# Performance work log

Measured on AMD Instinct MI355X. Metric: run time of the kernel, lower is better.

## Reference

```python
import jax, jax.numpy as jnp
import numpy as np

B, N, D = 4, 4096, 512          # batch, seq_len, hidden_size
H, DH = 8, 64                    # n_heads, head_dim
M = 512                          # nb_features = 0.125 * seq_len
LN_EPS = 1e-12
KERNEL_EPS = 1e-4


def setup_inputs() -> dict:
    key = jax.random.key(0)
    ks = jax.random.split(key, 12)
    s = 0.02
    return {
        "input_tensor": jax.random.normal(ks[0], (B, N, D), jnp.float32),
        "attention_mask": jnp.zeros((B, 1, 1, N), jnp.float32),  # unused by module
        "Wq": jax.random.normal(ks[1], (D, D), jnp.float32) * s,
        "bq": jnp.zeros((D,), jnp.float32),
        "Wk": jax.random.normal(ks[2], (D, D), jnp.float32) * s,
        "bk": jnp.zeros((D,), jnp.float32),
        "Wv": jax.random.normal(ks[3], (D, D), jnp.float32) * s,
        "bv": jnp.zeros((D,), jnp.float32),
        # gaussian (orthogonal-style) random feature projections [M, DH]
        "proj_q": jax.random.normal(ks[4], (M, DH), jnp.float32),
        "proj_k": jax.random.normal(ks[5], (M, DH), jnp.float32),
        "Wd": jax.random.normal(ks[6], (D, D), jnp.float32) * s,
        "bd": jnp.zeros((D,), jnp.float32),
        "gamma": jnp.ones((D,), jnp.float32),
        "beta": jnp.zeros((D,), jnp.float32),
    }


def _softmax_kernel(data, projection_matrix, is_query):
    # data: [B,H,N,DH], projection_matrix: [M,DH]
    data_normalizer = data.shape[-1] ** (-0.25)
    ratio = projection_matrix.shape[0] ** (-0.5)
    data_dash = jnp.einsum("bhnd,md->bhnm", data_normalizer * data, projection_matrix)
    diag_data = (jnp.sum(data * data, axis=-1) * 0.5 * data_normalizer ** 2)[..., None]
    if is_query:
        stab = jnp.max(data_dash, axis=-1, keepdims=True)
    else:
        stab = jnp.max(data_dash)  # global max, per original code
    return ratio * (jnp.exp(data_dash - diag_data - stab) + KERNEL_EPS)


def _linear_attention(q, k, v):
    # q,k: [B,H,N,M]; v: [B,H,N,DH]
    k_cumsum = jnp.sum(k, axis=-2)                               # [B,H,M]
    d_inv = 1.0 / jnp.einsum("bhnm,bhm->bhn", q, k_cumsum)       # [B,H,N]
    context = jnp.einsum("bhnm,bhne->bhme", k, v)                # [B,H,M,DH]
    return jnp.einsum("bhme,bhnm,bhn->bhne", context, q, d_inv)  # [B,H,N,DH]


def reference(input_tensor, attention_mask, Wq, bq, Wk, bk, Wv, bv,
              proj_q, proj_k, Wd, bd, gamma, beta):
    def heads(x):  # [B,N,D] -> [B,H,N,DH]
        return x.reshape(B, N, H, DH).transpose(0, 2, 1, 3)

    q = heads(input_tensor @ Wq.T + bq)
    k = heads(input_tensor @ Wk.T + bk)
    v = heads(input_tensor @ Wv.T + bv)

    q = _softmax_kernel(q, proj_q, is_query=True)
    k = _softmax_kernel(k, proj_k, is_query=False)

    ctx = _linear_attention(q, k, v)                  # [B,H,N,DH]
    ctx = ctx.transpose(0, 2, 1, 3).reshape(B, N, D)  # merge heads

    hidden = ctx @ Wd.T + bd                          # dropout is identity (eval)
    x = hidden + input_tensor
    mu = jnp.mean(x, axis=-1, keepdims=True)
    var = jnp.mean((x - mu) ** 2, axis=-1, keepdims=True)
    return (x - mu) / jnp.sqrt(var + LN_EPS) * gamma + beta
```

## Files before the change

### kernel.cpp

```cpp
#include <hip/hip_runtime.h>
#include <math.h>

typedef __bf16 bf16;
typedef __bf16 bf16x8 __attribute__((ext_vector_type(8)));
typedef __bf16 bf16x4 __attribute__((ext_vector_type(4)));
typedef float  f32x4  __attribute__((ext_vector_type(4)));

#define NSEQ 4096
#define DMODEL 512
#define DHEAD 64
#define MFEAT 512
#define BHEADS 32
#define ROWS_TOTAL 16384

#define NORMALIZER 0.35355339059327373f
#define DIAG_C 0.0625f
#define KEPS 1e-4f

__device__ __forceinline__ float warpReduceSum(float v) {
#pragma unroll
    for (int off = 32; off > 0; off >>= 1) v += __shfl_xor(v, off);
    return v;
}

__device__ __forceinline__ void atomicMaxF(float* addr, float val) {
    int* ai = (int*)addr;
    int cur = __float_as_int(*addr);
    while (__int_as_float(cur) < val) {
        int prev = atomicCAS(ai, cur, __float_as_int(val));
        if (prev == cur) break;
        cur = prev;
    }
}

__device__ __forceinline__ void gload16(const void* g, void* l) {
    __builtin_amdgcn_global_load_lds((const __attribute__((address_space(1))) void*)g,
                                     (__attribute__((address_space(3))) void*)l, 16, 0, 0);
}

__global__ __launch_bounds__(256)
void prep_convert(const float* __restrict__ x, const float* __restrict__ Wq,
                  const float* __restrict__ Wk, const float* __restrict__ Wv,
                  const float* __restrict__ Wd, const float* __restrict__ pq,
                  const float* __restrict__ bq, const float* __restrict__ bk,
                  const float* __restrict__ bv,
                  bf16* __restrict__ xb, bf16* __restrict__ Wb,
                  bf16* __restrict__ Wdb, bf16* __restrict__ pqb,
                  float* __restrict__ bcat)
{
    size_t i4 = (size_t)blockIdx.x * 256 + threadIdx.x;
    size_t e0 = i4 * 4;
    if (e0 >= 9471488) return;
    const float* src;
    if (e0 < 8388608) {
        src = x + e0;
        float4 v = *(const float4*)src;
        bf16* d = xb + e0;
        d[0] = (bf16)v.x; d[1] = (bf16)v.y; d[2] = (bf16)v.z; d[3] = (bf16)v.w;
    } else if (e0 < 9175040) {
        size_t c = e0 - 8388608; int wsel = (int)(c >> 18); size_t o = c & 262143;
        src = (wsel == 0 ? Wq : wsel == 1 ? Wk : Wv) + o;
        float4 v = *(const float4*)src;
        bf16* d = Wb + c;
        d[0] = (bf16)v.x; d[1] = (bf16)v.y; d[2] = (bf16)v.z; d[3] = (bf16)v.w;
    } else if (e0 < 9437184) {
        size_t c = e0 - 9175040;
        src = Wd + c;
        float4 v = *(const float4*)src;
        bf16* d = Wdb + c;
        d[0] = (bf16)v.x; d[1] = (bf16)v.y; d[2] = (bf16)v.z; d[3] = (bf16)v.w;
    } else if (e0 < 9469952) {
        size_t c = e0 - 9437184;
        src = pq + c;
        float4 v = *(const float4*)src;
        const int feat = (int)(c >> 6), col = (int)(c & 63);
        bf16x4 d4;
        d4[0] = (bf16)v.x; d4[1] = (bf16)v.y; d4[2] = (bf16)v.z; d4[3] = (bf16)v.w;
        const int inrow = (col << 1) ^ ((feat & 7) << 4);
        *(bf16x4*)((char*)pqb + (size_t)feat * 128 + inrow) = d4;
    } else {
        size_t c = e0 - 9469952; int wsel = (int)(c >> 9); size_t o = c & 511;
        src = (wsel == 0 ? bq : wsel == 1 ? bk : bv) + o;
        *(float4*)(bcat + c) = *(const float4*)src;
    }
}

template<int MODE>
__global__ __launch_bounds__(256)
void gemm_mfma(const bf16* __restrict__ A, const bf16* __restrict__ Bw,
               const float* __restrict__ bias, const float* __restrict__ resid,
               bf16* __restrict__ outQ, bf16* __restrict__ outK,
               bf16* __restrict__ outV, float* __restrict__ outF)
{
    __shared__ char As[16384];
    __shared__ char Bs[16384];
    const int tid = threadIdx.x;
    const int w = tid >> 6, l = tid & 63;
    const int wr = w >> 1, wc = w & 1;
    const int row0 = blockIdx.y << 7;
    const int col0 = blockIdx.x << 7;

    f32x4 acc[4][4] = {};
    const char* Ab = (const char*)A + (size_t)row0 * 1024;
    const char* Bb = (const char*)Bw + (size_t)col0 * 1024;

    for (int kt = 0; kt < 8; ++kt) {
        const int k0b = kt << 7;
#pragma unroll
        for (int i = 0; i < 4; ++i) {
            int off = (i << 12) + (tid << 4);
            int g = off ^ ((off >> 3) & 0x70);
            int grow = g >> 7, gcol = g & 127;
            gload16(Ab + (size_t)grow * 1024 + k0b + gcol, As + (i << 12) + (w << 10));
            gload16(Bb + (size_t)grow * 1024 + k0b + gcol, Bs + (i << 12) + (w << 10));
        }
        __syncthreads();
#pragma unroll
        for (int ks = 0; ks < 2; ++ks) {
            bf16x8 af[4], bb[4];
#pragma unroll
            for (int mi = 0; mi < 4; ++mi) {
                int row = (wr << 6) + (mi << 4) + (l & 15);
                int addr = ((row << 7) + (ks << 6) + ((l >> 4) << 4)) ^ ((row & 7) << 4);
                af[mi] = *(const bf16x8*)(As + addr);
            }
#pragma unroll
            for (int nj = 0; nj < 4; ++nj) {
                int row = (wc << 6) + (nj << 4) + (l & 15);
                int addr = ((row << 7) + (ks << 6) + ((l >> 4) << 4)) ^ ((row & 7) << 4);
                bb[nj] = *(const bf16x8*)(Bs + addr);
            }
#pragma unroll
            for (int mi = 0; mi < 4; ++mi)
#pragma unroll
                for (int nj = 0; nj < 4; ++nj)
                    acc[mi][nj] = __builtin_amdgcn_mfma_f32_16x16x32_bf16(af[mi], bb[nj], acc[mi][nj], 0, 0, 0);
        }
        __syncthreads();
    }

    const int subrow = (l >> 4) << 2;
    const int subcol = l & 15;
#pragma unroll
    for (int mi = 0; mi < 4; ++mi) {
#pragma unroll
        for (int nj = 0; nj < 4; ++nj) {
            const int cg = col0 + (wc << 6) + (nj << 4) + subcol;
            const float bi = bias[cg];
            const int rgb = row0 + (wr << 6) + (mi << 4) + subrow;
            if (MODE == 0) {
                if (cg < 512) {
                    const int hh = cg >> 6, ee = cg & 63;
                    const int bb2 = rgb >> 12, n = rgb & 4095;
#pragma unroll
                    for (int r = 0; r < 4; ++r)
                        outQ[((size_t)((bb2 * 8 + hh) * 4096 + n + r)) * 64 + ee] =
                            (bf16)(acc[mi][nj][r] + bi);
                } else if (cg < 1024) {
                    const int eg = cg - 512, hh = eg >> 6, ee = eg & 63;
#pragma unroll
                    for (int r = 0; r < 4; ++r) {
                        const int rg = rgb + r;
                        *(bf16*)((char*)outK + (size_t)rg * 1024 + hh * 128 +
                                 ((ee * 2) ^ ((rg & 7) << 4))) = (bf16)(acc[mi][nj][r] + bi);
                    }
                } else {
                    const int eg = cg - 1024, hh = eg >> 6, ee = eg & 63;
                    const int bb2 = rgb >> 12, n = rgb & 4095;
                    bf16x4 pv;
#pragma unroll
                    for (int r = 0; r < 4; ++r) pv[r] = (bf16)(acc[mi][nj][r] + bi);
                    const int nb = n * 2;
                    size_t byteaddr = (size_t)((bb2 * 8 + hh) * 64 + ee) * 8192
                                    + (size_t)((nb & ~127) | ((nb & 127) ^ ((ee & 7) << 4)));
                    *(bf16x4*)((char*)outV + byteaddr) = pv;
                }
            } else {
#pragma unroll
                for (int r = 0; r < 4; ++r) {
                    const int rg = rgb + r;
                    outF[(size_t)rg * 512 + cg] = acc[mi][nj][r] + bi + resid[(size_t)rg * 512 + cg];
                }
            }
        }
    }
}

__global__ __launch_bounds__(64)
void vsum_kernel(const bf16* __restrict__ Vt, float* __restrict__ vsum)
{
    const int row = blockIdx.x;
    const bf16x8* p = (const bf16x8*)((const char*)Vt + (size_t)row * 8192);
    float s = 0.f;
#pragma unroll
    for (int i = 0; i < 8; ++i) {
        bf16x8 v = p[threadIdx.x + i * 64];
#pragma unroll
        for (int u = 0; u < 8; ++u) s += (float)v[u];
    }
    s = warpReduceSum(s);
    if (threadIdx.x == 0) vsum[row] = s;
}

__global__ __launch_bounds__(256)
void diag_kernel(const bf16* __restrict__ Kb, float* __restrict__ dgk)
{
    const int idx = blockIdx.x * 256 + threadIdx.x;
    const int bh = idx >> 12, n = idx & 4095;
    const int b = bh >> 3, h = bh & 7;
    const char* row = (const char*)Kb + (size_t)(b * 4096 + n) * 1024 + h * 128;
    const int sw = (n & 7) << 4;
    float ss = 0.f;
#pragma unroll
    for (int j = 0; j < 8; ++j) {
        bf16x8 v = *(const bf16x8*)(row + ((j << 4) ^ sw));
#pragma unroll
        for (int u = 0; u < 8; ++u) { float f = (float)v[u]; ss += f * f; }
    }
    dgk[idx] = DIAG_C * ss;
}

__global__ __launch_bounds__(256)
void kside_mfma4(const bf16* __restrict__ Kb, const bf16* __restrict__ Vt,
                 const float* __restrict__ projk, const float* __restrict__ dgk,
                 float* __restrict__ ctxp8, float* __restrict__ esumf8,
                 float* __restrict__ gmax)
{
    const int tid = threadIdx.x;
    const int w = tid >> 6, l = tid & 63;
    const int lq = l & 15, lg = l >> 4;
    const int bh = blockIdx.x;
    const int b = bh >> 3, h = bh & 7;
    const int M0w = (blockIdx.y << 7) + (w << 5);
    const int z = blockIdx.z;
    const int nbase = z << 9;

    bf16x8 pk[2][2];
#pragma unroll
    for (int mj = 0; mj < 2; ++mj)
#pragma unroll
        for (int ks = 0; ks < 2; ++ks) {
            const int m = M0w + (mj << 4) + lq;
            const float* p = projk + (size_t)m * 64 + (ks << 5) + (lg << 3);
            float4 a = *(const float4*)p;
            float4 c = *(const float4*)(p + 4);
            bf16x8 f;
            f[0] = (bf16)a.x; f[1] = (bf16)a.y; f[2] = (bf16)a.z; f[3] = (bf16)a.w;
            f[4] = (bf16)c.x; f[5] = (bf16)c.y; f[6] = (bf16)c.z; f[7] = (bf16)c.w;
            pk[mj][ks] = f;
        }

    const char* kgb = (const char*)Kb + (size_t)(b * 4096) * 1024 + h * 128;
    const char* vgb = (const char*)Vt + (size_t)bh * 64 * 8192;
    const float* dgb = dgk + bh * 4096;
    const int swl = (lq & 7) << 4;

    f32x4 acc2[4][2] = {};
    float esacc[2] = {0.f, 0.f};
    float lmax = -1e30f;
    const f32x4 Zc = {0.f, 0.f, 0.f, 0.f};

    for (int c = 0; c < 4; ++c) {
#pragma unroll
        for (int g = 0; g < 4; ++g) {
            const int nA = nbase + (c << 7) + (g << 5);
            bf16x8 afA[2], afB[2];
            {
                const char* pA = kgb + (size_t)(nA + lq) * 1024;
#pragma unroll
                for (int ks = 0; ks < 2; ++ks) {
                    const int off = ((ks << 6) + (lg << 4)) ^ swl;
                    afA[ks] = *(const bf16x8*)(pA + off);
                    afB[ks] = *(const bf16x8*)(pA + 16384 + off);
                }
            }
            bf16x8 av[4];
#pragma unroll
            for (int et = 0; et < 4; ++et) {
                const int e = (et << 4) + lq;
                av[et] = *(const bf16x8*)(vgb + (size_t)e * 8192 +
                           ((((nA + (lg << 3)) << 1)) ^ swl));
            }
            float4 dgA = *(const float4*)(dgb + nA + (lg << 2));
            float4 dgB = *(const float4*)(dgb + nA + 16 + (lg << 2));
            const float dgAr[4] = {dgA.x, dgA.y, dgA.z, dgA.w};
            const float dgBr[4] = {dgB.x, dgB.y, dgB.z, dgB.w};
            f32x4 dA[2], dB[2];
#pragma unroll
            for (int mj = 0; mj < 2; ++mj) {
                dA[mj] = __builtin_amdgcn_mfma_f32_16x16x32_bf16(afA[0], pk[mj][0], Zc, 0, 0, 0);
                dA[mj] = __builtin_amdgcn_mfma_f32_16x16x32_bf16(afA[1], pk[mj][1], dA[mj], 0, 0, 0);
                dB[mj] = __builtin_amdgcn_mfma_f32_16x16x32_bf16(afB[0], pk[mj][0], Zc, 0, 0, 0);
                dB[mj] = __builtin_amdgcn_mfma_f32_16x16x32_bf16(afB[1], pk[mj][1], dB[mj], 0, 0, 0);
            }
#pragma unroll
            for (int mj = 0; mj < 2; ++mj) {
                float eA[4], eB[4];
#pragma unroll
                for (int r = 0; r < 4; ++r) {
                    const float kdA = NORMALIZER * dA[mj][r];
                    const float kdB = NORMALIZER * dB[mj][r];
                    lmax = fmaxf(lmax, fmaxf(kdA, kdB));
                    eA[r] = __expf(kdA - dgAr[r]);
                    eB[r] = __expf(kdB - dgBr[r]);
                    esacc[mj] += eA[r] + eB[r];
                }
                unsigned int wA0, wA1, wB0, wB1;
                asm("v_cvt_pk_bf16_f32 %0, %1, %2" : "=v"(wA0) : "v"(eA[0]), "v"(eA[1]));
                asm("v_cvt_pk_bf16_f32 %0, %1, %2" : "=v"(wA1) : "v"(eA[2]), "v"(eA[3]));
                asm("v_cvt_pk_bf16_f32 %0, %1, %2" : "=v"(wB0) : "v"(eB[0]), "v"(eB[1]));
                asm("v_cvt_pk_bf16_f32 %0, %1, %2" : "=v"(wB1) : "v"(eB[2]), "v"(eB[3]));
                const int selE = (l >= 32) ? (int)wB0 : (int)wA0;
                const int selO = (l >= 32) ? (int)wB1 : (int)wA1;
                const int base = ((l & 16) << 1) + lq;
                unsigned int w0 = (unsigned int)__shfl(selE, base);
                unsigned int w1 = (unsigned int)__shfl(selO, base);
                unsigned int w2 = (unsigned int)__shfl(selE, base + 16);
                unsigned int w3 = (unsigned int)__shfl(selO, base + 16);
                union { unsigned int u[4]; bf16x8 v; } bfr;
                bfr.u[0] = w0; bfr.u[1] = w1; bfr.u[2] = w2; bfr.u[3] = w3;
#pragma unroll
                for (int et = 0; et < 4; ++et)
                    acc2[et][mj] = __builtin_amdgcn_mfma_f32_16x16x32_bf16(
                        av[et], bfr.v, acc2[et][mj], 0, 0, 0);
            }
        }
    }

#pragma unroll
    for (int mj = 0; mj < 2; ++mj) {
        float s = esacc[mj];
        s += __shfl_xor(s, 16); s += __shfl_xor(s, 32);
        if (l < 16)
            esumf8[((size_t)z * 32 + bh) * 512 + M0w + (mj << 4) + lq] = s;
    }
#pragma unroll
    for (int off = 32; off > 0; off >>= 1) lmax = fmaxf(lmax, __shfl_xor(lmax, off));
    if (l == 0) atomicMaxF(gmax, lmax);

    float* cz = ctxp8 + (size_t)z * (32 * 64 * 512) + (size_t)bh * 64 * 512;
#pragma unroll
    for (int et = 0; et < 4; ++et)
#pragma unroll
        for (int mj = 0; mj < 2; ++mj)
#pragma unroll
            for (int r = 0; r < 4; ++r) {
                const int e = (et << 4) + (lg << 2) + r;
                cz[(size_t)e * 512 + M0w + (mj << 4) + lq] = acc2[et][mj][r];
            }
}

__global__ __launch_bounds__(256)
void finalize_ctx(const float* __restrict__ ctxp8, const float* __restrict__ esumf8,
                  bf16* __restrict__ ctxE, float* __restrict__ ctxsum,
                  float* __restrict__ esumsum)
{
    __shared__ float red_s[4][64];
    const int tid = threadIdx.x;
    const int bh = blockIdx.x;
    const int mc = blockIdx.y << 7;
    const int e = tid & 63, ms = tid >> 6;
    const size_t Z = (size_t)32 * 64 * 512;

    const float* cb = ctxp8 + (size_t)bh * 64 * 512 + (size_t)e * 512 + mc + (ms << 5);
    char* obr = (char*)ctxE + ((size_t)bh * 80 + e) * 1024;
    float s = 0.f;
#pragma unroll
    for (int i8 = 0; i8 < 4; ++i8) {
        float acc[8] = {};
#pragma unroll
        for (int zz = 0; zz < 8; ++zz) {
            float4 v0 = *(const float4*)(cb + zz * Z + (i8 << 3));
            float4 v1 = *(const float4*)(cb + zz * Z + (i8 << 3) + 4);
            acc[0] += v0.x; acc[1] += v0.y; acc[2] += v0.z; acc[3] += v0.w;
            acc[4] += v1.x; acc[5] += v1.y; acc[6] += v1.z; acc[7] += v1.w;
        }
        bf16x8 p8;
#pragma unroll
        for (int u = 0; u < 8; ++u) { s += acc[u]; p8[u] = (bf16)acc[u]; }
        const int mloc = mc + (ms << 5) + (i8 << 3);
        *(bf16x8*)(obr + ((mloc << 1) ^ ((e & 7) << 4))) = p8;
    }
    red_s[ms][e] = s;
    __syncthreads();
    if (tid < 64)
        atomicAdd(ctxsum + bh * 64 + tid,
                  red_s[0][tid] + red_s[1][tid] + red_s[2][tid] + red_s[3][tid]);
    if (tid < 128) {
        const int m = mc + tid;
        float ev = 0.f;
#pragma unroll
        for (int zz = 0; zz < 8; ++zz)
            ev += esumf8[((size_t)zz * 32 + bh) * 512 + m];
        bf16* er = ctxE + (size_t)(bh * 80 + 64) * 512;
        er[m] = (bf16)1.0f;
        er[512 + (m ^ 8)] = (bf16)ev;
        float t = warpReduceSum(ev);
        if ((tid & 63) == 0) atomicAdd(esumsum + bh, t);
    }
}

__global__ __launch_bounds__(512, 1)
void qside_mfma4(const bf16* __restrict__ Qb, const bf16* __restrict__ Pq,
                 const bf16* __restrict__ CtxE, const float* __restrict__ vsum,
                 const float* __restrict__ ctxsum, const float* __restrict__ esumsum,
                 const float* __restrict__ gmax, bf16* __restrict__ OutC)
{
    __shared__ char ctx_s[81920];
    __shared__ char pq_s[2][16384];
    __shared__ char T_s[40960];

    const int tid = threadIdx.x;
    const int w = tid >> 6, l = tid & 63;
    const int lq = l & 15, lg = l >> 4;
    const int bh = blockIdx.x;
    const int b = bh >> 3, h = bh & 7;
    const int n0 = blockIdx.y << 9;

    const char* ctxg = (const char*)CtxE + (size_t)bh * 81920;
    const char* pqg  = (const char*)Pq;
#pragma unroll
    for (int i = 0; i < 10; ++i)
        gload16(ctxg + (i << 13) + (tid << 4), ctx_s + (i << 13) + (w << 10));
#pragma unroll
    for (int p = 0; p < 2; ++p)
        gload16(pqg + (p << 13) + (tid << 4), pq_s[0] + (p << 13) + (w << 10));

    const char* qgb = (const char*)Qb + ((size_t)bh * 4096 + n0 + (w << 6)) * 128;
    bf16x8 qa[4][2];
    float diag_l[4];
#pragma unroll
    for (int ni = 0; ni < 4; ++ni) {
        const char* qr = qgb + ((ni << 4) + lq) * 128;
        float ss = 0.f;
#pragma unroll
        for (int kk = 0; kk < 2; ++kk) {
            qa[ni][kk] = *(const bf16x8*)(qr + (kk << 6) + (lg << 4));
#pragma unroll
            for (int u = 0; u < 8; ++u) { float f = (float)qa[ni][kk][u]; ss += f * f; }
        }
        ss += __shfl_xor(ss, 16);
        ss += __shfl_xor(ss, 32);
        diag_l[ni] = DIAG_C * ss;
    }

    f32x4 acc2[4][5] = {};
    float mmax[4] = {-1e30f, -1e30f, -1e30f, -1e30f};
    char* tw = T_s + w * 5120;
    const f32x4 Zc = {0.f, 0.f, 0.f, 0.f};

    __syncthreads();

    for (int ft = 0; ft < 4; ++ft) {
        const int buf = ft & 1;
        if (ft < 3) {
#pragma unroll
            for (int p = 0; p < 2; ++p)
                gload16(pqg + ((ft + 1) << 14) + (p << 13) + (tid << 4),
                        pq_s[buf ^ 1] + (p << 13) + (w << 10));
        }
        const char* pqb = pq_s[buf];
#pragma unroll
        for (int sl = 0; sl < 4; ++sl) {
            f32x4 acc1[2][4];
#pragma unroll
            for (int mi = 0; mi < 2; ++mi) {
                const int fr = (sl << 5) + (mi << 4) + lq;
                bf16x8 pf = *(const bf16x8*)(pqb + fr * 128 +
                              (((lg << 4)) ^ ((lq & 7) << 4)));
#pragma unroll
                for (int ni = 0; ni < 4; ++ni)
                    acc1[mi][ni] = __builtin_amdgcn_mfma_f32_16x16x32_bf16(pf, qa[ni][0], Zc, 0, 0, 0);
            }
#pragma unroll
            for (int mi = 0; mi < 2; ++mi) {
                const int fr = (sl << 5) + (mi << 4) + lq;
                bf16x8 pf = *(const bf16x8*)(pqb + fr * 128 +
                              ((64 + (lg << 4)) ^ ((lq & 7) << 4)));
#pragma unroll
                for (int ni = 0; ni < 4; ++ni)
                    acc1[mi][ni] = __builtin_amdgcn_mfma_f32_16x16x32_bf16(pf, qa[ni][1], acc1[mi][ni], 0, 0, 0);
            }
#pragma unroll
            for (int mi = 0; mi < 2; ++mi)
#pragma unroll
                for (int ni = 0; ni < 4; ++ni) {
                    bf16x4 tv;
#pragma unroll
                    for (int r = 0; r < 4; ++r) {
                        const float qd = acc1[mi][ni][r];
                        mmax[ni] = fmaxf(mmax[ni], qd);
                        tv[r] = (bf16)__expf(NORMALIZER * qd - diag_l[ni]);
                    }
                    *(bf16x4*)(tw + ((ni << 4) + lq) * 80 + (mi << 5) + (lg << 3)) = tv;
                }
            bf16x8 ta[4];
#pragma unroll
            for (int ni = 0; ni < 4; ++ni)
                ta[ni] = *(const bf16x8*)(tw + ((ni << 4) + lq) * 80 + (lg << 4));
#pragma unroll
            for (int nj = 0; nj < 5; ++nj) {
                const int e = (nj << 4) + lq;
                bf16x8 cb = *(const bf16x8*)(ctx_s + e * 1024 +
                              (((ft << 8) + (sl << 6) + (lg << 4)) ^ ((e & 7) << 4)));
#pragma unroll
                for (int ni = 0; ni < 4; ++ni)
                    acc2[ni][nj] = __builtin_amdgcn_mfma_f32_16x16x32_bf16(ta[ni], cb, acc2[ni][nj], 0, 0, 0);
            }
        }
        __syncthreads();
    }

    const float sG = __expf(-gmax[0]);
    const float ess = esumsum[bh];
    bf16* outb = OutC + ((size_t)(b * 4096) + n0 + (w << 6)) * 512 + (h << 6);
#pragma unroll
    for (int ni = 0; ni < 4; ++ni) {
        float mmr = mmax[ni];
        mmr = fmaxf(mmr, __shfl_xor(mmr, 16));
        mmr = fmaxf(mmr, __shfl_xor(mmr, 32));
#pragma unroll
        for (int r = 0; r < 4; ++r) {
            const float mm = __shfl(mmr, (lg << 2) + r);
            const float uT = __shfl(acc2[ni][4][r], (lg << 4));
            const float uE = __shfl(acc2[ni][4][r], (lg << 4) | 1);
            const float cr = __expf(-NORMALIZER * mm);
            const float qsum = cr * uT + KEPS * 512.0f;
            const float D = sG * (cr * uE + KEPS * ess) + KEPS * 4096.0f * qsum;
            const float inv = 1.0f / D;
            const float al = sG * cr * inv;
            const float G1 = sG * KEPS * inv;
            const float G2 = KEPS * qsum * inv;
            const int row = (ni << 4) + (lg << 2) + r;
#pragma unroll
            for (int nj = 0; nj < 4; ++nj) {
                const int e = (nj << 4) + lq;
                float v = al * acc2[ni][nj][r] + G1 * ctxsum[(bh << 6) + e] + G2 * vsum[(bh << 6) + e];
                outb[(size_t)row * 512 + e] = (bf16)v;
            }
        }
    }
}

__global__ __launch_bounds__(256)
void ln_kernel(const float* __restrict__ hid, const float* __restrict__ gamma,
               const float* __restrict__ beta, float* __restrict__ out)
{
    const int row = (blockIdx.x << 2) + (threadIdx.x >> 6);
    const int lane = threadIdx.x & 63;
    const float* x = hid + (size_t)row * DMODEL + (lane << 3);
    float4 a = *(const float4*)x;
    float4 c = *(const float4*)(x + 4);
    float s = a.x + a.y + a.z + a.w + c.x + c.y + c.z + c.w;
    float sq = a.x * a.x + a.y * a.y + a.z * a.z + a.w * a.w +
               c.x * c.x + c.y * c.y + c.z * c.z + c.w * c.w;
    s = warpReduceSum(s);
    sq = warpReduceSum(sq);
    const float mu = s * 0.001953125f;
    const float var = sq * 0.001953125f - mu * mu;
    const float rs = rsqrtf(var + 1e-12f);
    const float4 g1 = *(const float4*)(gamma + (lane << 3));
    const float4 g2 = *(const float4*)(gamma + (lane << 3) + 4);
    const float4 b1 = *(const float4*)(beta + (lane << 3));
    const float4 b2 = *(const float4*)(beta + (lane << 3) + 4);
    float4 o1, o2;
    o1.x = (a.x - mu) * rs * g1.x + b1.x;
    o1.y = (a.y - mu) * rs * g1.y + b1.y;
    o1.z = (a.z - mu) * rs * g1.z + b1.z;
    o1.w = (a.w - mu) * rs * g1.w + b1.w;
    o2.x = (c.x - mu) * rs * g2.x + b2.x;
    o2.y = (c.y - mu) * rs * g2.y + b2.y;
    o2.z = (c.z - mu) * rs * g2.z + b2.z;
    o2.w = (c.w - mu) * rs * g2.w + b2.w;
    *(float4*)(out + (size_t)row * DMODEL + (lane << 3)) = o1;
    *(float4*)(out + (size_t)row * DMODEL + (lane << 3) + 4) = o2;
}

__global__ void init_misc(float* gmax)
{
    if (threadIdx.x == 0 && blockIdx.x == 0) *gmax = -1e30f;
}

extern "C" void kernel_launch(void* const* d_in, const int* in_sizes, int n_in,
                              void* d_out, int out_size, void* d_ws, size_t ws_size,
                              hipStream_t stream)
{
    const float* x     = (const float*)d_in[0];
    const float* Wq    = (const float*)d_in[2];
    const float* bq    = (const float*)d_in[3];
    const float* Wk    = (const float*)d_in[4];
    const float* bk    = (const float*)d_in[5];
    const float* Wv    = (const float*)d_in[6];
    const float* bv    = (const float*)d_in[7];
    const float* projq = (const float*)d_in[8];
    const float* projk = (const float*)d_in[9];
    const float* Wd    = (const float*)d_in[10];
    const float* bd    = (const float*)d_in[11];
    const float* gamma = (const float*)d_in[12];
    const float* beta  = (const float*)d_in[13];

    char* W = (char*)d_ws;
    bf16*  qb16   = (bf16*) (W);
    bf16*  kb16s  = (bf16*) (W + 16777216);
    bf16*  vtb    = (bf16*) (W + 33554432);
    bf16*  xb16   = (bf16*) (W + 50331648);
    float* hidf32 = (float*)(W + 67108864);
    float* ctxp8  = (float*)(W + 67108864);
    float* esumf8 = (float*)(W + 100663296);
    float* dgk    = (float*)(W + 101187584);
    bf16*  Wb16   = (bf16*) (W + 100663296);
    bf16*  Wdb16  = (bf16*) (W + 102236160);
    bf16*  pqb16  = (bf16*) (W + 102760448);
    float* bcat   = (float*)(W + 102825984);
    bf16*  ctxE   = (bf16*) (W + 102832128);
    float* vsumb  = (float*)(W + 105453568);
    float* ctxsum = (float*)(W + 105461760);
    float* esmsm  = (float*)(W + 105469952);
    float* gmaxb  = (float*)(W + 105470080);

    prep_convert<<<9250, 256, 0, stream>>>(x, Wq, Wk, Wv, Wd, projq, bq, bk, bv,
                                           xb16, Wb16, Wdb16, pqb16, bcat);
    hipMemsetAsync(ctxE, 0, 2621440, stream);
    hipMemsetAsync(ctxsum, 0, 8192 + 128, stream);
    init_misc<<<1, 64, 0, stream>>>(gmaxb);

    gemm_mfma<0><<<dim3(12, 128), 256, 0, stream>>>(xb16, Wb16, bcat, nullptr,
                                                    qb16, kb16s, vtb, nullptr);

    diag_kernel<<<512, 256, 0, stream>>>(kb16s, dgk);
    vsum_kernel<<<2048, 64, 0, stream>>>(vtb, vsumb);
    kside_mfma4<<<dim3(32, 4, 8), 256, 0, stream>>>(kb16s, vtb, projk, dgk,
                                                    ctxp8, esumf8, gmaxb);
    finalize_ctx<<<dim3(32, 4), 256, 0, stream>>>(ctxp8, esumf8, ctxE, ctxsum, esmsm);

    qside_mfma4<<<dim3(32, 8), 512, 0, stream>>>(qb16, pqb16, ctxE, vsumb,
                                                 ctxsum, esmsm, gmaxb, xb16);

    gemm_mfma<1><<<dim3(4, 128), 256, 0, stream>>>(xb16, Wdb16, bd, x,
                                                   nullptr, nullptr, nullptr, hidf32);
    ln_kernel<<<4096, 256, 0, stream>>>(hidf32, gamma, beta, (float*)d_out);
}
```

Before: 218.5 us.

## Stage K/V tiles in LDS with double buffering in k-side kernel

The k-side feature/context kernel now uses 512-thread blocks covering 256 features. Each block cooperatively loads 64-row K and V chunks into double-buffered shared memory, so all eight waves share the tiles instead of each wave loading them from global memory. The exp results are written to per-wave LDS tiles rather than rearranged with cross-lane shuffles. The sequence split drops from 8 to 4 partitions, which halves the partial buffers the finalize pass has to reduce. In exchange there are per-chunk barriers, much more LDS per block, and fewer blocks in flight.

```diff
diff --git a/kernel.cpp b/kernel.cpp
--- a/kernel.cpp
+++ b/kernel.cpp
@@ -220,27 +220,31 @@
     dgk[idx] = DIAG_C * ss;
 }
 
-__global__ __launch_bounds__(256)
-void kside_mfma4(const bf16* __restrict__ Kb, const bf16* __restrict__ Vt,
+__global__ __launch_bounds__(512, 1)
+void kside_mfma6(const bf16* __restrict__ Kb, const bf16* __restrict__ Vt,
                  const float* __restrict__ projk, const float* __restrict__ dgk,
-                 float* __restrict__ ctxp8, float* __restrict__ esumf8,
+                 float* __restrict__ ctxp4, float* __restrict__ esumf4,
                  float* __restrict__ gmax)
 {
+    __shared__ char K_s[16384];
+    __shared__ char V_s[16384];
+    __shared__ char E_s[32768];
+
     const int tid = threadIdx.x;
     const int w = tid >> 6, l = tid & 63;
     const int lq = l & 15, lg = l >> 4;
     const int bh = blockIdx.x;
     const int b = bh >> 3, h = bh & 7;
-    const int M0w = (blockIdx.y << 7) + (w << 5);
+    const int mw = (blockIdx.y << 8) + (w << 5);
     const int z = blockIdx.z;
-    const int nbase = z << 9;
+    const int swl = (lq & 7) << 4;
 
     bf16x8 pk[2][2];
 #pragma unroll
     for (int mj = 0; mj < 2; ++mj)
 #pragma unroll
         for (int ks = 0; ks < 2; ++ks) {
-            const int m = M0w + (mj << 4) + lq;
+            const int m = mw + (mj << 4) + lq;
             const float* p = projk + (size_t)m * 64 + (ks << 5) + (lg << 3);
             float4 a = *(const float4*)p;
             float4 c = *(const float4*)(p + 4);
@@ -252,79 +256,85 @@
 
     const char* kgb = (const char*)Kb + (size_t)(b * 4096) * 1024 + h * 128;
     const char* vgb = (const char*)Vt + (size_t)bh * 64 * 8192;
-    const float* dgb = dgk + bh * 4096;
-    const int swl = (lq & 7) << 4;
+    const float* dgb = dgk + (bh << 12);
+    const int trow = tid >> 3;
+    const int tseg = (tid & 7) << 4;
+    char* tw = E_s + (w << 12);
 
     f32x4 acc2[4][2] = {};
     float esacc[2] = {0.f, 0.f};
     float lmax = -1e30f;
     const f32x4 Zc = {0.f, 0.f, 0.f, 0.f};
 
-    for (int c = 0; c < 4; ++c) {
-#pragma unroll
-        for (int g = 0; g < 4; ++g) {
-            const int nA = nbase + (c << 7) + (g << 5);
-            bf16x8 afA[2], afB[2];
-            {
-                const char* pA = kgb + (size_t)(nA + lq) * 1024;
-#pragma unroll
-                for (int ks = 0; ks < 2; ++ks) {
-                    const int off = ((ks << 6) + (lg << 4)) ^ swl;
-                    afA[ks] = *(const bf16x8*)(pA + off);
-                    afB[ks] = *(const bf16x8*)(pA + 16384 + off);
+    {
+        const int nc = z << 10;
+        gload16(kgb + (size_t)(nc + trow) * 1024 + tseg, K_s + (tid << 4));
+        gload16(vgb + (size_t)trow * 8192 + (nc << 1) + tseg, V_s + (tid << 4));
+    }
+
+    int cur = 0;
+    for (int c = 0; c < 16; ++c) {
+        __syncthreads();
+        if (c < 15) {
+            const int nn = (z << 10) + ((c + 1) << 6);
+            gload16(kgb + (size_t)(nn + trow) * 1024 + tseg,
+                    K_s + ((cur ^ 1) << 13) + (tid << 4));
+            gload16(vgb + (size_t)trow * 8192 + (nn << 1) + tseg,
+                    V_s + ((cur ^ 1) << 13) + (tid << 4));
+        }
+        const char* Kc = K_s + (cur << 13);
+        const char* Vc = V_s + (cur << 13);
+        const int nc = (z << 10) + (c << 6);
+
+        f32x4 acc1[4][2];
+#pragma unroll
+        for (int nt = 0; nt < 4; ++nt) {
+            const char* kr = Kc + ((nt << 4) + lq) * 128;
+            bf16x8 afk0 = *(const bf16x8*)(kr + ((lg << 4) ^ swl));
+            bf16x8 afk1 = *(const bf16x8*)(kr + ((64 + (lg << 4)) ^ swl));
+#pragma unroll
+            for (int mj = 0; mj < 2; ++mj) {
+                acc1[nt][mj] = __builtin_amdgcn_mfma_f32_16x16x32_bf16(afk0, pk[mj][0], Zc, 0, 0, 0);
+                acc1[nt][mj] = __builtin_amdgcn_mfma_f32_16x16x32_bf16(afk1, pk[mj][1], acc1[nt][mj], 0, 0, 0);
+            }
+        }
+#pragma unroll
+        for (int nt = 0; nt < 4; ++nt) {
+            float4 dv = *(const float4*)(dgb + nc + (nt << 4) + (lg << 2));
+            const float dgr[4] = {dv.x, dv.y, dv.z, dv.w};
+#pragma unroll
+            for (int mj = 0; mj < 2; ++mj) {
+                const int m = (mj << 4) + lq;
+                bf16x4 ev;
+#pragma unroll
+                for (int r = 0; r < 4; ++r) {
+                    float kd = NORMALIZER * acc1[nt][mj][r];
+                    lmax = fmaxf(lmax, kd);
+                    float e = __expf(kd - dgr[r]);
+                    esacc[mj] += e;
+                    ev[r] = (bf16)e;
                 }
-            }
-            bf16x8 av[4];
+                *(bf16x4*)(tw + m * 128 + (((nt << 5) + (lg << 3)) ^ swl)) = ev;
+            }
+        }
+#pragma unroll
+        for (int ks2 = 0; ks2 < 2; ++ks2) {
+            bf16x8 be[2];
+#pragma unroll
+            for (int mj = 0; mj < 2; ++mj) {
+                const int m = (mj << 4) + lq;
+                be[mj] = *(const bf16x8*)(tw + m * 128 + (((ks2 << 6) + (lg << 4)) ^ swl));
+            }
 #pragma unroll
             for (int et = 0; et < 4; ++et) {
                 const int e = (et << 4) + lq;
-                av[et] = *(const bf16x8*)(vgb + (size_t)e * 8192 +
-                           ((((nA + (lg << 3)) << 1)) ^ swl));
-            }
-            float4 dgA = *(const float4*)(dgb + nA + (lg << 2));
-            float4 dgB = *(const float4*)(dgb + nA + 16 + (lg << 2));
-            const float dgAr[4] = {dgA.x, dgA.y, dgA.z, dgA.w};
-            const float dgBr[4] = {dgB.x, dgB.y, dgB.z, dgB.w};
-            f32x4 dA[2], dB[2];
-#pragma unroll
-            for (int mj = 0; mj < 2; ++mj) {
-                dA[mj] = __builtin_amdgcn_mfma_f32_16x16x32_bf16(afA[0], pk[mj][0], Zc, 0, 0, 0);
-                dA[mj] = __builtin_amdgcn_mfma_f32_16x16x32_bf16(afA[1], pk[mj][1], dA[mj], 0, 0, 0);
-                dB[mj] = __builtin_amdgcn_mfma_f32_16x16x32_bf16(afB[0], pk[mj][0], Zc, 0, 0, 0);
-                dB[mj] = __builtin_amdgcn_mfma_f32_16x16x32_bf16(afB[1], pk[mj][1], dB[mj], 0, 0, 0);
-            }
-#pragma unroll
-            for (int mj = 0; mj < 2; ++mj) {
-                float eA[4], eB[4];
-#pragma unroll
-                for (int r = 0; r < 4; ++r) {
-                    const float kdA = NORMALIZER * dA[mj][r];
-                    const float kdB = NORMALIZER * dB[mj][r];
-                    lmax = fmaxf(lmax, fmaxf(kdA, kdB));
-                    eA[r] = __expf(kdA - dgAr[r]);
-                    eB[r] = __expf(kdB - dgBr[r]);
-                    esacc[mj] += eA[r] + eB[r];
-                }
-                unsigned int wA0, wA1, wB0, wB1;
-                asm("v_cvt_pk_bf16_f32 %0, %1, %2" : "=v"(wA0) : "v"(eA[0]), "v"(eA[1]));
-                asm("v_cvt_pk_bf16_f32 %0, %1, %2" : "=v"(wA1) : "v"(eA[2]), "v"(eA[3]));
-                asm("v_cvt_pk_bf16_f32 %0, %1, %2" : "=v"(wB0) : "v"(eB[0]), "v"(eB[1]));
-                asm("v_cvt_pk_bf16_f32 %0, %1, %2" : "=v"(wB1) : "v"(eB[2]), "v"(eB[3]));
-                const int selE = (l >= 32) ? (int)wB0 : (int)wA0;
-                const int selO = (l >= 32) ? (int)wB1 : (int)wA1;
-                const int base = ((l & 16) << 1) + lq;
-                unsigned int w0 = (unsigned int)__shfl(selE, base);
-                unsigned int w1 = (unsigned int)__shfl(selO, base);
-                unsigned int w2 = (unsigned int)__shfl(selE, base + 16);
-                unsigned int w3 = (unsigned int)__shfl(selO, base + 16);
-                union { unsigned int u[4]; bf16x8 v; } bfr;
-                bfr.u[0] = w0; bfr.u[1] = w1; bfr.u[2] = w2; bfr.u[3] = w3;
-#pragma unroll
-                for (int et = 0; et < 4; ++et)
-                    acc2[et][mj] = __builtin_amdgcn_mfma_f32_16x16x32_bf16(
-                        av[et], bfr.v, acc2[et][mj], 0, 0, 0);
-            }
-        }
+                bf16x8 av = *(const bf16x8*)(Vc + e * 128 + (((ks2 << 6) + (lg << 4)) ^ swl));
+#pragma unroll
+                for (int mj = 0; mj < 2; ++mj)
+                    acc2[et][mj] = __builtin_amdgcn_mfma_f32_16x16x32_bf16(av, be[mj], acc2[et][mj], 0, 0, 0);
+            }
+        }
+        cur ^= 1;
     }
 
 #pragma unroll
@@ -332,13 +342,13 @@
         float s = esacc[mj];
         s += __shfl_xor(s, 16); s += __shfl_xor(s, 32);
         if (l < 16)
-            esumf8[((size_t)z * 32 + bh) * 512 + M0w + (mj << 4) + lq] = s;
+            esumf4[((size_t)z * 32 + bh) * 512 + mw + (mj << 4) + lq] = s;
     }
 #pragma unroll
     for (int off = 32; off > 0; off >>= 1) lmax = fmaxf(lmax, __shfl_xor(lmax, off));
     if (l == 0) atomicMaxF(gmax, lmax);
 
-    float* cz = ctxp8 + (size_t)z * (32 * 64 * 512) + (size_t)bh * 64 * 512;
+    float* cz = ctxp4 + (size_t)z * (32 * 64 * 512) + (size_t)bh * 64 * 512;
 #pragma unroll
     for (int et = 0; et < 4; ++et)
 #pragma unroll
@@ -346,12 +356,12 @@
 #pragma unroll
             for (int r = 0; r < 4; ++r) {
                 const int e = (et << 4) + (lg << 2) + r;
-                cz[(size_t)e * 512 + M0w + (mj << 4) + lq] = acc2[et][mj][r];
+                cz[(size_t)e * 512 + mw + (mj << 4) + lq] = acc2[et][mj][r];
             }
 }
 
 __global__ __launch_bounds__(256)
-void finalize_ctx(const float* __restrict__ ctxp8, const float* __restrict__ esumf8,
+void finalize_ctx(const float* __restrict__ ctxp4, const float* __restrict__ esumf4,
                   bf16* __restrict__ ctxE, float* __restrict__ ctxsum,
                   float* __restrict__ esumsum)
 {
@@ -362,14 +372,14 @@
     const int e = tid & 63, ms = tid >> 6;
     const size_t Z = (size_t)32 * 64 * 512;
 
-    const float* cb = ctxp8 + (size_t)bh * 64 * 512 + (size_t)e * 512 + mc + (ms << 5);
+    const float* cb = ctxp4 + (size_t)bh * 64 * 512 + (size_t)e * 512 + mc + (ms << 5);
     char* obr = (char*)ctxE + ((size_t)bh * 80 + e) * 1024;
     float s = 0.f;
 #pragma unroll
     for (int i8 = 0; i8 < 4; ++i8) {
         float acc[8] = {};
 #pragma unroll
-        for (int zz = 0; zz < 8; ++zz) {
+        for (int zz = 0; zz < 4; ++zz) {
             float4 v0 = *(const float4*)(cb + zz * Z + (i8 << 3));
             float4 v1 = *(const float4*)(cb + zz * Z + (i8 << 3) + 4);
             acc[0] += v0.x; acc[1] += v0.y; acc[2] += v0.z; acc[3] += v0.w;
@@ -388,10 +398,10 @@
                   red_s[0][tid] + red_s[1][tid] + red_s[2][tid] + red_s[3][tid]);
     if (tid < 128) {
         const int m = mc + tid;
-        float ev = 0.f;
-#pragma unroll
-        for (int zz = 0; zz < 8; ++zz)
-            ev += esumf8[((size_t)zz * 32 + bh) * 512 + m];
+        float ev = esumf4[(size_t)bh * 512 + m]
+                 + esumf4[((size_t)32 + bh) * 512 + m]
+                 + esumf4[((size_t)64 + bh) * 512 + m]
+                 + esumf4[((size_t)96 + bh) * 512 + m];
         bf16* er = ctxE + (size_t)(bh * 80 + 64) * 512;
         er[m] = (bf16)1.0f;
         er[512 + (m ^ 8)] = (bf16)ev;
@@ -605,9 +615,9 @@
     bf16*  vtb    = (bf16*) (W + 33554432);
     bf16*  xb16   = (bf16*) (W + 50331648);
     float* hidf32 = (float*)(W + 67108864);
-    float* ctxp8  = (float*)(W + 67108864);
-    float* esumf8 = (float*)(W + 100663296);
-    float* dgk    = (float*)(W + 101187584);
+    float* ctxp4  = (float*)(W + 67108864);
+    float* esumf4 = (float*)(W + 83886080);
+    float* dgk    = (float*)(W + 84148224);
     bf16*  Wb16   = (bf16*) (W + 100663296);
     bf16*  Wdb16  = (bf16*) (W + 102236160);
     bf16*  pqb16  = (bf16*) (W + 102760448);
@@ -629,9 +639,9 @@
 
     diag_kernel<<<512, 256, 0, stream>>>(kb16s, dgk);
     vsum_kernel<<<2048, 64, 0, stream>>>(vtb, vsumb);
-    kside_mfma4<<<dim3(32, 4, 8), 256, 0, stream>>>(kb16s, vtb, projk, dgk,
-                                                    ctxp8, esumf8, gmaxb);
-    finalize_ctx<<<dim3(32, 4), 256, 0, stream>>>(ctxp8, esumf8, ctxE, ctxsum, esmsm);
+    kside_mfma6<<<dim3(32, 2, 4), 512, 0, stream>>>(kb16s, vtb, projk, dgk,
+                                                    ctxp4, esumf4, gmaxb);
+    finalize_ctx<<<dim3(32, 4), 256, 0, stream>>>(ctxp4, esumf4, ctxE, ctxsum, esmsm);
 
     qside_mfma4<<<dim3(32, 8), 512, 0, stream>>>(qb16, pqb16, ctxE, vsumb,
                                                  ctxsum, esmsm, gmaxb, xb16);
```

After: 199.8 us. 1.09x faster.
